# Kernel optimization log

Hardware: AMD Instinct MI355X
Metric: run time of the kernel (lower is better)

The kernel has to match this reference:

```python
import jax, jax.numpy as jnp
import numpy as np

B, L, DIM = 8, 512, 8          # batch, seq len, raw channels (value dim D = 2*DIM = 16)
ET, HID, H = 128, 128, 2       # embed_time, hidden_size, num_heads
MAXLEN = 512
NEG = -1e9


def setup_inputs() -> dict:
    key = jax.random.key(0)
    ks = jax.random.split(key, 40)
    def n(i, shape, s=0.05):
        return jax.random.normal(ks[i], shape, jnp.float32) * s
    vals = jax.random.normal(ks[0], (B, L, DIM), jnp.float32)
    msk = (jax.random.uniform(ks[1], (B, L, DIM)) > 0.2).astype(jnp.float32)
    x = jnp.concatenate([vals, msk], -1)                      # (B, L, 2*DIM)
    time_steps = jax.random.uniform(ks[2], (B, L), jnp.float32)
    return {
        'x': x, 'time_steps': time_steps,
        # learned time embedding: Linear(1, ET-1) periodic + Linear(1,1)
        'w_per': n(3, (1, ET - 1)), 'b_per': n(4, (ET - 1,)),
        'w_lin': n(5, (1, 1)), 'b_lin': n(6, (1,)),
        # MultiTimeAttention projections
        'Wq_t': n(7, (ET, ET)), 'bq_t': n(8, (ET,)),
        'Wk_t': n(9, (ET, ET)), 'bk_t': n(10, (ET,)),
        'Wo_t': n(11, (2 * DIM * H, HID)), 'bo_t': n(12, (HID,)),
        'pos_emb': n(13, (MAXLEN + 1, HID)), 'cls_emb': n(14, (1, HID)),
        # transformer block (BERT-style post-LN encoder layer, d_ff=HID)
        'tWq': n(15, (HID, HID)), 'tbq': n(16, (HID,)),
        'tWk': n(17, (HID, HID)), 'tbk': n(18, (HID,)),
        'tWv': n(19, (HID, HID)), 'tbv': n(20, (HID,)),
        'tWo': n(21, (HID, HID)), 'tbo': n(22, (HID,)),
        'ln1_g': jnp.ones((HID,), jnp.float32), 'ln1_b': jnp.zeros((HID,), jnp.float32),
        'fW1': n(23, (HID, HID)), 'fb1': n(24, (HID,)),
        'fW2': n(25, (HID, HID)), 'fb2': n(26, (HID,)),
        'ln2_g': jnp.ones((HID,), jnp.float32), 'ln2_b': jnp.zeros((HID,), jnp.float32),
        # BertPooler
        'pW': n(27, (HID, HID)), 'pb': n(28, (HID,)),
    }


def _time_emb(tt, w_per, b_per, w_lin, b_lin):
    tt = tt[..., None]                                        # (B, L, 1)
    return jnp.concatenate([tt @ w_lin + b_lin, jnp.sin(tt @ w_per + b_per)], -1)


def _ln(x, g, b, eps=1e-5):
    m = x.mean(-1, keepdims=True)
    v = ((x - m) ** 2).mean(-1, keepdims=True)
    return (x - m) / jnp.sqrt(v + eps) * g + b


def _mta(q_emb, k_emb, value, mask, Wq, bq, Wk, bk, Wo, bo):
    # MultiTimeAttention: scores broadcast to value-channel axis, softmax over keys
    D = value.shape[-1]
    dk = ET // H
    def split(e, W, b):
        p = e @ W + b
        return p.reshape(e.shape[0], -1, H, dk).transpose(0, 2, 1, 3)
    q = split(q_emb, Wq, bq)                                  # (Bq, H, Lq, dk)
    k = split(k_emb, Wk, bk)                                  # (B,  H, Lk, dk)
    scores = jnp.matmul(q, k.swapaxes(-1, -2)) / jnp.sqrt(jnp.float32(dk))  # (B,H,Lq,Lk)
    s5 = jnp.where(mask[:, None, None, :, :] == 0, NEG, scores[..., None])  # (B,H,Lq,Lk,D)
    p = jax.nn.softmax(s5, axis=-2)
    out = jnp.einsum('bhqkd,bkd->bhqd', p, value)             # (B, H, Lq, D)
    Bv = value.shape[0]
    out = out.transpose(0, 2, 1, 3).reshape(Bv, -1, H * D)
    return out @ Wo + bo


def _tblock(x, tWq, tbq, tWk, tbk, tWv, tbv, tWo, tbo, ln1_g, ln1_b,
            fW1, fb1, fW2, fb2, ln2_g, ln2_b):
    Bq, Lq, _ = x.shape
    dk = HID // H
    def heads(W, b):
        return (x @ W + b).reshape(Bq, Lq, H, dk).transpose(0, 2, 1, 3)
    q, k, v = heads(tWq, tbq), heads(tWk, tbk), heads(tWv, tbv)
    a = jax.nn.softmax(jnp.matmul(q, k.swapaxes(-1, -2)) / jnp.sqrt(jnp.float32(dk)), -1)
    o = jnp.matmul(a, v).transpose(0, 2, 1, 3).reshape(Bq, Lq, HID) @ tWo + tbo
    x = _ln(x + o, ln1_g, ln1_b)
    f = jax.nn.relu(x @ fW1 + fb1) @ fW2 + fb2
    return _ln(x + f, ln2_g, ln2_b)


def reference(x, time_steps, w_per, b_per, w_lin, b_lin,
              Wq_t, bq_t, Wk_t, bk_t, Wo_t, bo_t, pos_emb, cls_emb,
              tWq, tbq, tWk, tbk, tWv, tbv, tWo, tbo, ln1_g, ln1_b,
              fW1, fb1, fW2, fb2, ln2_g, ln2_b, pW, pb):
    Bx = x.shape[0]
    mask_half = x[:, :, DIM:]
    mask = jnp.concatenate([mask_half, mask_half], -1)        # (B, L, 2*DIM)
    key_e = _time_emb(time_steps, w_per, b_per, w_lin, b_lin)
    tq_e = _time_emb(time_steps, w_per, b_per, w_lin, b_lin)  # query_time_steps=None -> same
    cls_t = jnp.linspace(0.0, 1.0, 128, dtype=jnp.float32)[None]
    cls_q_e = _time_emb(cls_t, w_per, b_per, w_lin, b_lin)    # (1, 128, ET)
    cls_out = _mta(cls_q_e, key_e, x, mask, Wq_t, bq_t, Wk_t, bk_t, Wo_t, bo_t)
    out = _mta(tq_e, key_e, x, mask, Wq_t, bq_t, Wk_t, bk_t, Wo_t, bo_t)
    tb = (tWq, tbq, tWk, tbk, tWv, tbv, tWo, tbo, ln1_g, ln1_b,
          fW1, fb1, fW2, fb2, ln2_g, ln2_b)
    cls_repr = jnp.broadcast_to(cls_emb[None, :, :], (Bx, 1, HID))
    # encode(cls_out, is_pooling=True), pooling='bert': no pos emb, take token 0
    h = _tblock(jnp.concatenate([cls_repr, cls_out], 1), *tb)
    cls_pooling = jnp.tanh(h[:, 0] @ pW + pb)                 # (B, HID)
    # encode(out, is_pooling=False) [pretrain path]: pos emb + transformer, drop CLS
    h2 = jnp.concatenate([cls_repr, out], 1)                  # (B, L+1, HID)
    h2 = h2 + pos_emb[:h2.shape[1]][None]
    h2 = _tblock(h2, *tb)
    last_hidden_state = h2[:, 1:]                             # (B, L, HID)
    return cls_pooling, last_hidden_state
```

## Files before the change

kernel.cpp:

```cpp
#include <hip/hip_runtime.h>
#include <hip/hip_bf16.h>
#include <math.h>


static constexpr int NM_ = 8 * 513;
static constexpr int NC_ = 8 * 129;
static constexpr int NT_ = NM_ + NC_;

using bf = __hip_bfloat16;
typedef __attribute__((ext_vector_type(8))) short bf16x8;
typedef __attribute__((ext_vector_type(4))) short bf16x4;
typedef __attribute__((ext_vector_type(4))) float floatx4;
typedef __attribute__((ext_vector_type(8))) unsigned short ushortx8;

__device__ __forceinline__ float wave_reduce_sum(float v) {
    #pragma unroll
    for (int off = 32; off >= 1; off >>= 1) v += __shfl_xor(v, off);
    return v;
}
__device__ __forceinline__ float wave_reduce_max(float v) {
    #pragma unroll
    for (int off = 32; off >= 1; off >>= 1) v = fmaxf(v, __shfl_xor(v, off));
    return v;
}
__device__ __forceinline__ float u2f(unsigned short u) {
    return __uint_as_float(((unsigned)u) << 16);
}
__device__ __forceinline__ unsigned short f2u(float f) {
    unsigned u = __float_as_uint(f);
    return (unsigned short)((u + 0x7FFF + ((u >> 16) & 1)) >> 16);
}
__device__ __forceinline__ bf16x8 join8(bf16x4 lo, bf16x4 hi) {
    return __builtin_shufflevector(lo, hi, 0, 1, 2, 3, 4, 5, 6, 7);
}
__device__ __forceinline__ float rdin(const void* p, int i, int flag) {
    return flag ? u2f(((const unsigned short*)p)[i]) : ((const float*)p)[i];
}

struct PrepAll {
    const void* src[32]; int n[32]; int dstoff[32];
    int cstart[32]; int cnum[32];
    int ncv;
    const void* wsrc[8]; unsigned short* wdst[8]; float wscale[8];
    const void* ts; const void* w_per; const void* b_per;
    const void* w_lin; const void* b_lin;
    unsigned short* key_e16;
    unsigned short* btg;
    const void* xsrc;
    const unsigned short* det;
};
__global__ void prep_all_kernel(PrepAll a, float* dst) {
    int flag = (a.det[0] == 0x3F80u) ? 1 : 0;
    int blk = blockIdx.x, tid = threadIdx.x;
    if (blk < a.ncv) {
        int which = -1, bi = 0;
        #pragma unroll
        for (int i = 0; i < 32; ++i)
            if (blk >= a.cstart[i] && blk < a.cstart[i] + a.cnum[i]) { which = i; bi = blk - a.cstart[i]; }
        if (which < 0) return;
        int i = bi * 256 + tid;
        if (i < a.n[which]) dst[a.dstoff[which] + i] = rdin(a.src[which], i, flag);
    } else if (blk < a.ncv + 512) {
        int p = blk - a.ncv;
        int m = p >> 6;
        int idx = (p & 63) * 256 + tid;
        int c = idx >> 9;
        int l = (idx >> 3) & 63;
        int j = idx & 7;
        int k = (c >> 3) * 32 + (l >> 4) * 8 + j;
        int n = (c & 7) * 16 + (l & 15);
        a.wdst[m][idx] = f2u(rdin(a.wsrc[m], k * 128 + n, flag) * a.wscale[m]);
    } else if (blk < a.ncv + 512 + 2112) {
        int p = blk - a.ncv - 512;
        int row = p * 2 + (tid >> 7), j = tid & 127;
        float t = (row < 4096) ? rdin(a.ts, row, flag)
                               : (float)(row - 4096) * (1.0f / 127.0f);
        float v;
        if (j == 0) v = t * rdin(a.w_lin, 0, flag) + rdin(a.b_lin, 0, flag);
        else        v = sinf(t * rdin(a.w_per, j - 1, flag) + rdin(a.b_per, j - 1, flag));
        a.key_e16[row * 128 + j] = f2u(v);
    } else {
        int p = blk - a.ncv - 512 - 2112;
        int e0 = (p * 256 + tid) * 8;
        int b = e0 >> 13;
        int c = (e0 >> 9) & 15;
        int k0 = e0 & 511;
        unsigned short out[8];
        #pragma unroll
        for (int j = 0; j < 8; ++j) {
            int k = k0 + j;
            float m = rdin(a.xsrc, (b * 512 + k) * 16 + 8 + (c & 7), flag);
            float val = (c < 8) ? rdin(a.xsrc, (b * 512 + k) * 16 + c, flag) * m : m;
            out[j] = f2u(val);
        }
        *(ushortx8*)(a.btg + e0) = *(ushortx8*)out;
    }
}

struct GemmM {
    const void* A[3]; const unsigned short* W[3]; const float* bias[3];
    unsigned short* C[3];
    int M[3]; float bscale[3];
};
__global__ void __launch_bounds__(256)
gemm_mfma_kernel(GemmM p) {
    int y = blockIdx.y;
    const unsigned short* Wsw = p.W[y];
    const float* bias = p.bias[y];
    unsigned short* C = p.C[y];
    int M = p.M[y];
    float bscale = p.bscale[y];
    int m0 = blockIdx.x * 16;
    if (m0 >= M) return;
    __shared__ unsigned short As[16][136];
    int tid = threadIdx.x;
    {
        const unsigned short* A = (const unsigned short*)p.A[y];
        int r = tid >> 4, c0 = (tid & 15) * 8;
        ushortx8 v = {0, 0, 0, 0, 0, 0, 0, 0};
        if (m0 + r < M) v = *(const ushortx8*)(A + (size_t)(m0 + r) * 128 + c0);
        *(ushortx8*)&As[r][c0] = v;
    }
    __syncthreads();

    int wv = tid >> 6, lane = tid & 63;
    floatx4 acc0 = {0.f, 0.f, 0.f, 0.f}, acc1 = acc0;
    int am = lane & 15, aq = lane >> 4;
    #pragma unroll
    for (int ks = 0; ks < 4; ++ks) {
        bf16x8 af = *(bf16x8*)&As[am][ks * 32 + aq * 8];
        const unsigned short* base = Wsw + ((size_t)ks * 8 + 2 * wv) * 512 + lane * 8;
        bf16x8 b0 = *(const bf16x8*)(base);
        bf16x8 b1 = *(const bf16x8*)(base + 512);
        acc0 = __builtin_amdgcn_mfma_f32_16x16x32_bf16(af, b0, acc0, 0, 0, 0);
        acc1 = __builtin_amdgcn_mfma_f32_16x16x32_bf16(af, b1, acc1, 0, 0, 0);
    }
    int col = lane & 15, rowb = (lane >> 4) * 4;
    #pragma unroll
    for (int t = 0; t < 2; ++t) {
        floatx4 acc = t ? acc1 : acc0;
        int n = wv * 32 + t * 16 + col;
        float bv = bias[n] * bscale;
        #pragma unroll
        for (int rg = 0; rg < 4; ++rg) {
            int m = m0 + rowb + rg;
            if (m < M) C[(size_t)m * 128 + n] = f2u(acc[rg] + bv);
        }
    }
}

__global__ void __launch_bounds__(256)
mta_att_kernel(const unsigned short* qp_cls, const unsigned short* qp_main,
               const unsigned short* kp, const unsigned short* btg,
               float* att_cls, float* att_mn) {
    int F = blockIdx.x;
    int b = F & 7;
    int j = F >> 3;
    int h = j & 1;
    int xx = j >> 1;
    int is_cls = (xx >= 32);
    int qt = is_cls ? (xx - 32) : xx;
    int tid = threadIdx.x, lane = tid & 63, wv = tid >> 6;
    __shared__ unsigned short Qs[16][72];
    __shared__ unsigned short KV[64][72];
    __shared__ unsigned short sp[16][520];
    int q0 = qt * 16;

    if (tid < 128) {
        int r = tid >> 3, c0 = (tid & 7) * 8;
        const unsigned short* qrow = is_cls ? (qp_cls + (size_t)(q0 + r) * 128 + h * 64)
                                            : (qp_main + (size_t)(b * 512 + q0 + r) * 128 + h * 64);
        *(ushortx8*)&Qs[r][c0] = *(const ushortx8*)(qrow + c0);
    }
    __syncthreads();

    bf16x8 qf0, qf1;
    {
        int m = lane & 15, g = lane >> 4;
        qf0 = *(const bf16x8*)&Qs[m][g * 8];
        qf1 = *(const bf16x8*)&Qs[m][32 + g * 8];
    }

    for (int kt = 0; kt < 8; ++kt) {
        int k0 = kt * 64;
        {
            int kk = tid >> 3, e0 = (tid & 7) * 8;
            #pragma unroll
            for (int it = 0; it < 2; ++it, kk += 32)
                *(ushortx8*)&KV[kk][e0] =
                    *(const ushortx8*)(kp + (size_t)(b * 512 + k0 + kk) * 128 + h * 64 + e0);
        }
        __syncthreads();
        int kn = lane & 15, g = lane >> 4;
        floatx4 acc = {0.f, 0.f, 0.f, 0.f};
        {
            bf16x8 b0 = *(const bf16x8*)&KV[wv * 16 + kn][g * 8];
            acc = __builtin_amdgcn_mfma_f32_16x16x32_bf16(qf0, b0, acc, 0, 0, 0);
            bf16x8 b1 = *(const bf16x8*)&KV[wv * 16 + kn][32 + g * 8];
            acc = __builtin_amdgcn_mfma_f32_16x16x32_bf16(qf1, b1, acc, 0, 0, 0);
        }
        int colk = k0 + wv * 16 + kn;
        #pragma unroll
        for (int rg = 0; rg < 4; ++rg) sp[g * 4 + rg][colk] = f2u(acc[rg]);
        __syncthreads();
    }

    for (int rr = wv; rr < 16; rr += 4) {
        float m = -1e30f;
        for (int k = lane; k < 512; k += 64) m = fmaxf(m, u2f(sp[rr][k]));
        m = wave_reduce_max(m);
        for (int k = lane; k < 512; k += 64) sp[rr][k] = f2u(expf(u2f(sp[rr][k]) - m));
    }
    __syncthreads();

    floatx4 macc = {0.f, 0.f, 0.f, 0.f};
    {
        int mq = lane & 15, g = lane >> 4;
        const unsigned short* bbase = btg + ((size_t)(b * 16 + mq)) * 512 + g * 8;
        #pragma unroll
        for (int cc = 0; cc < 4; ++cc) {
            int koff = (wv + cc * 4) * 32;
            bf16x8 af = *(const bf16x8*)&sp[mq][koff + g * 8];
            bf16x8 bfv = *(const bf16x8*)(bbase + koff);
            macc = __builtin_amdgcn_mfma_f32_16x16x32_bf16(af, bfv, macc, 0, 0, 0);
        }
    }
    float* redC = (float*)&KV[0][0];
    float* Cfull = redC + 1024;
    #pragma unroll
    for (int rg = 0; rg < 4; ++rg) redC[(wv * 64 + lane) * 4 + rg] = macc[rg];
    __syncthreads();
    {
        int l = tid >> 2, rg = tid & 3;
        float s = redC[l * 4 + rg] + redC[(64 + l) * 4 + rg]
                + redC[(128 + l) * 4 + rg] + redC[(192 + l) * 4 + rg];
        int row = (l >> 4) * 4 + rg, c = l & 15;
        Cfull[row * 16 + c] = s;
    }
    __syncthreads();
    if (tid < 128) {
        int r = tid >> 3, c = tid & 7;
        float num = Cfull[r * 16 + c];
        float den = Cfull[r * 16 + 8 + c];
        int row = q0 + r;
        float* dst = is_cls ? (att_cls + (size_t)(b * 128 + row) * 32)
                            : (att_mn + (size_t)(b * 512 + row) * 32);
        dst[h * 16 + c] = num / den;
        dst[h * 16 + 8 + c] = 1.0f;
    }
}

__global__ void __launch_bounds__(256)
mta_qkv_kernel(const float* att, const float* Wo, const float* bo,
               const float* cls_emb, const float* pos, float* xin,
               const unsigned short* Wq, const unsigned short* Wk, const unsigned short* Wv,
               const float* bq, const float* bk, const float* bv_,
               unsigned short* outq, unsigned short* outk, unsigned short* outv) {
    int m0 = blockIdx.x * 16;
    __shared__ float As32[16][36];
    __shared__ unsigned short As[16][136];
    int tid = threadIdx.x;
    int r = tid >> 4, g = tid & 15, c0 = g * 8;

    int R = m0 + r;
    int srow, prow;
    if (R < NM_) {
        int b = R / 513, rr = R - b * 513;
        srow = (rr == 0) ? -1 : 1024 + b * 512 + (rr - 1);
        prow = rr;
    } else {
        int mc = R - NM_;
        int b = mc / 129, rr = mc - b * 129;
        srow = (rr == 0) ? -1 : b * 128 + (rr - 1);
        prow = -1;
    }
    if (g < 2 && srow >= 0) {
        const float* src = att + (size_t)srow * 32 + g * 16;
        *(float4*)&As32[r][g * 16]      = *(const float4*)(src);
        *(float4*)&As32[r][g * 16 + 4]  = *(const float4*)(src + 4);
        *(float4*)&As32[r][g * 16 + 8]  = *(const float4*)(src + 8);
        *(float4*)&As32[r][g * 16 + 12] = *(const float4*)(src + 12);
    }
    __syncthreads();

    float acc[8];
    if (srow < 0) {
        #pragma unroll
        for (int j = 0; j < 8; ++j) acc[j] = cls_emb[c0 + j];
    } else {
        #pragma unroll
        for (int j = 0; j < 8; ++j) acc[j] = bo[c0 + j];
        #pragma unroll 8
        for (int k = 0; k < 32; ++k) {
            float a = As32[r][k];
            const float4 w0 = *(const float4*)(Wo + (size_t)k * 128 + c0);
            const float4 w1 = *(const float4*)(Wo + (size_t)k * 128 + c0 + 4);
            acc[0] = fmaf(a, w0.x, acc[0]); acc[1] = fmaf(a, w0.y, acc[1]);
            acc[2] = fmaf(a, w0.z, acc[2]); acc[3] = fmaf(a, w0.w, acc[3]);
            acc[4] = fmaf(a, w1.x, acc[4]); acc[5] = fmaf(a, w1.y, acc[5]);
            acc[6] = fmaf(a, w1.z, acc[6]); acc[7] = fmaf(a, w1.w, acc[7]);
        }
    }
    if (prow >= 0) {
        const float* pr = pos + (size_t)prow * 128 + c0;
        float4 p0 = *(const float4*)(pr);
        float4 p1 = *(const float4*)(pr + 4);
        acc[0] += p0.x; acc[1] += p0.y; acc[2] += p0.z; acc[3] += p0.w;
        acc[4] += p1.x; acc[5] += p1.y; acc[6] += p1.z; acc[7] += p1.w;
    }
    *(float4*)(xin + (size_t)R * 128 + c0) = make_float4(acc[0], acc[1], acc[2], acc[3]);
    *(float4*)(xin + (size_t)R * 128 + c0 + 4) = make_float4(acc[4], acc[5], acc[6], acc[7]);
    *(ushort4*)&As[r][c0] = make_ushort4(f2u(acc[0]), f2u(acc[1]), f2u(acc[2]), f2u(acc[3]));
    *(ushort4*)&As[r][c0 + 4] = make_ushort4(f2u(acc[4]), f2u(acc[5]), f2u(acc[6]), f2u(acc[7]));
    __syncthreads();

    int wv = tid >> 6, lane = tid & 63;
    int am = lane & 15, aq = lane >> 4;
    int col = lane & 15, rowb = (lane >> 4) * 4;
    const unsigned short* Ws[3] = {Wq, Wk, Wv};
    const float* bs[3] = {bq, bk, bv_};
    float bsc[3] = {0.125f, 1.f, 1.f};
    unsigned short* Cs[3] = {outq, outk, outv};
    #pragma unroll
    for (int y = 0; y < 3; ++y) {
        floatx4 acc0 = {0.f, 0.f, 0.f, 0.f}, acc1 = acc0;
        #pragma unroll
        for (int ks = 0; ks < 4; ++ks) {
            bf16x8 af = *(bf16x8*)&As[am][ks * 32 + aq * 8];
            const unsigned short* base = Ws[y] + ((size_t)ks * 8 + 2 * wv) * 512 + lane * 8;
            bf16x8 b0 = *(const bf16x8*)(base);
            bf16x8 b1 = *(const bf16x8*)(base + 512);
            acc0 = __builtin_amdgcn_mfma_f32_16x16x32_bf16(af, b0, acc0, 0, 0, 0);
            acc1 = __builtin_amdgcn_mfma_f32_16x16x32_bf16(af, b1, acc1, 0, 0, 0);
        }
        #pragma unroll
        for (int t = 0; t < 2; ++t) {
            floatx4 a2 = t ? acc1 : acc0;
            int n = wv * 32 + t * 16 + col;
            float bvv = bs[y][n] * bsc[y];
            #pragma unroll
            for (int rg = 0; rg < 4; ++rg)
                Cs[y][(size_t)(m0 + rowb + rg) * 128 + n] = f2u(a2[rg] + bvv);
        }
    }
}

__global__ void __launch_bounds__(256)
tb_att_kernel(const unsigned short* qp, const unsigned short* kp,
              const unsigned short* vp, unsigned short* outp) {
    int F = blockIdx.x;
    int b = F & 7;
    int j = F >> 3;
    int h = j & 1;
    int xx = j >> 1;
    int is_cls = (xx >= 33);
    int qt = is_cls ? xx - 33 : xx;
    int Lq = is_cls ? 129 : 513;
    int base = is_cls ? (4104 + b * 129) : (b * 513);
    int nkt = is_cls ? 3 : 9;
    int tid = threadIdx.x, lane = tid & 63, wv = tid >> 6;
    __shared__ unsigned short Qs[16][72];
    __shared__ unsigned short KV[64][72];
    __shared__ unsigned short sp[16][588];
    __shared__ float rinv[16];
    int q0 = qt * 16;

    if (tid < 128) {
        int r = tid >> 3, c0 = (tid & 7) * 8;
        int qr = q0 + r;
        ushortx8 v = {0, 0, 0, 0, 0, 0, 0, 0};
        if (qr < Lq) v = *(const ushortx8*)(qp + (size_t)(base + qr) * 128 + h * 64 + c0);
        *(ushortx8*)&Qs[r][c0] = v;
    }
    __syncthreads();

    bf16x8 qf0, qf1;
    {
        int m = lane & 15, g = lane >> 4;
        qf0 = *(const bf16x8*)&Qs[m][g * 8];
        qf1 = *(const bf16x8*)&Qs[m][32 + g * 8];
    }

    for (int kt = 0; kt < nkt; ++kt) {
        int k0 = kt * 64;
        {
            int kk = tid >> 3, e0 = (tid & 7) * 8;
            #pragma unroll
            for (int it = 0; it < 2; ++it, kk += 32) {
                int krow = k0 + kk;
                ushortx8 v = {0, 0, 0, 0, 0, 0, 0, 0};
                if (krow < Lq) v = *(const ushortx8*)(kp + (size_t)(base + krow) * 128 + h * 64 + e0);
                *(ushortx8*)&KV[kk][e0] = v;
            }
        }
        __syncthreads();
        int kn = lane & 15, g = lane >> 4;
        floatx4 acc = {0.f, 0.f, 0.f, 0.f};
        {
            bf16x8 b0 = *(const bf16x8*)&KV[wv * 16 + kn][g * 8];
            acc = __builtin_amdgcn_mfma_f32_16x16x32_bf16(qf0, b0, acc, 0, 0, 0);
            bf16x8 b1 = *(const bf16x8*)&KV[wv * 16 + kn][32 + g * 8];
            acc = __builtin_amdgcn_mfma_f32_16x16x32_bf16(qf1, b1, acc, 0, 0, 0);
        }
        int colk = k0 + wv * 16 + kn;
        #pragma unroll
        for (int rg = 0; rg < 4; ++rg)
            sp[g * 4 + rg][colk] = f2u((colk < Lq) ? acc[rg] : -1e30f);
        __syncthreads();
    }

    int kend = nkt * 64;
    for (int rr = wv; rr < 16; rr += 4) {
        float m = -1e30f;
        for (int k = lane; k < kend; k += 64) m = fmaxf(m, u2f(sp[rr][k]));
        m = wave_reduce_max(m);
        float sum = 0.f;
        for (int k = lane; k < kend; k += 64) {
            float e = expf(u2f(sp[rr][k]) - m);
            sp[rr][k] = f2u(e);
            sum += e;
        }
        sum = wave_reduce_sum(sum);
        if (lane == 0) rinv[rr] = 1.f / sum;
    }

    floatx4 oacc = {0.f, 0.f, 0.f, 0.f};
    for (int kt = 0; kt < nkt; ++kt) {
        int k0 = kt * 64;
        __syncthreads();
        {
            int kk = tid & 31, e0 = (tid >> 5) * 8;
            #pragma unroll
            for (int it = 0; it < 2; ++it, kk += 32) {
                int krow = k0 + kk;
                ushortx8 v = {0, 0, 0, 0, 0, 0, 0, 0};
                if (krow < Lq) v = *(const ushortx8*)(vp + (size_t)(base + krow) * 128 + h * 64 + e0);
                #pragma unroll
                for (int j2 = 0; j2 < 8; ++j2) KV[e0 + j2][kk] = v[j2];
            }
        }
        __syncthreads();
        int dn = lane & 15, g = lane >> 4;
        #pragma unroll
        for (int c = 0; c < 2; ++c) {
            bf16x4 plo = *(const bf16x4*)&sp[lane & 15][k0 + c * 32 + g * 8];
            bf16x4 phi = *(const bf16x4*)&sp[lane & 15][k0 + c * 32 + g * 8 + 4];
            bf16x8 vf = *(const bf16x8*)&KV[wv * 16 + dn][c * 32 + g * 8];
            oacc = __builtin_amdgcn_mfma_f32_16x16x32_bf16(join8(plo, phi), vf, oacc, 0, 0, 0);
        }
    }
    int dcol = wv * 16 + (lane & 15), g = lane >> 4;
    #pragma unroll
    for (int rg = 0; rg < 4; ++rg) {
        int q = g * 4 + rg;
        int qr = q0 + q;
        if (qr < Lq)
            outp[(size_t)(base + qr) * 128 + h * 64 + dcol] = f2u(oacc[rg] * rinv[q]);
    }
}

__global__ void __launch_bounds__(256)
attnout_ffn_kernel(const unsigned short* A, const unsigned short* Wao, const float* bao,
                   const float* resid, const float* g1, const float* b1ln,
                   const unsigned short* W1, const float* fb1,
                   const unsigned short* W2, const float* fb2,
                   const float* g2, const float* b2ln,
                   const float* pW, const float* pb, float* dout) {
    int m0 = blockIdx.x * 16;
    __shared__ unsigned short As[16][136];
    __shared__ float Xs[16][128];
    __shared__ unsigned short Hs[16][136];
    __shared__ float redS[4][4][4], redQ[4][4][4];
    __shared__ float smean[16], sinv[16];
    __shared__ float x2row[128];
    __shared__ int poolb;
    int tid = threadIdx.x;
    if (tid == 0) poolb = -1;
    {
        int r = tid >> 4, c0 = (tid & 15) * 8;
        *(ushortx8*)&As[r][c0] = *(const ushortx8*)(A + (size_t)(m0 + r) * 128 + c0);
    }
    __syncthreads();

    int wv = tid >> 6, lane = tid & 63;
    int am = lane & 15, aq = lane >> 4;
    int col = lane & 15, g = lane >> 4, rowb = g * 4;

    float ov[2][4];
    {
        floatx4 acc0 = {0.f, 0.f, 0.f, 0.f}, acc1 = acc0;
        #pragma unroll
        for (int ks = 0; ks < 4; ++ks) {
            bf16x8 af = *(bf16x8*)&As[am][ks * 32 + aq * 8];
            const unsigned short* base = Wao + ((size_t)ks * 8 + 2 * wv) * 512 + lane * 8;
            bf16x8 bb0 = *(const bf16x8*)(base);
            bf16x8 bb1 = *(const bf16x8*)(base + 512);
            acc0 = __builtin_amdgcn_mfma_f32_16x16x32_bf16(af, bb0, acc0, 0, 0, 0);
            acc1 = __builtin_amdgcn_mfma_f32_16x16x32_bf16(af, bb1, acc1, 0, 0, 0);
        }
        #pragma unroll
        for (int t = 0; t < 2; ++t) {
            int n = wv * 32 + t * 16 + col;
            float bv = bao[n];
            floatx4 acc = t ? acc1 : acc0;
            #pragma unroll
            for (int rg = 0; rg < 4; ++rg)
                ov[t][rg] = acc[rg] + bv + resid[(size_t)(m0 + rowb + rg) * 128 + n];
        }
    }
    #pragma unroll
    for (int rg = 0; rg < 4; ++rg) {
        float s = ov[0][rg] + ov[1][rg];
        float q = ov[0][rg] * ov[0][rg] + ov[1][rg] * ov[1][rg];
        #pragma unroll
        for (int off = 8; off >= 1; off >>= 1) {
            s += __shfl_xor(s, off);
            q += __shfl_xor(q, off);
        }
        if ((lane & 15) == 0) { redS[wv][g][rg] = s; redQ[wv][g][rg] = q; }
    }
    __syncthreads();
    if (tid < 16) {
        int gg = tid >> 2, rg = tid & 3;
        float s = redS[0][gg][rg] + redS[1][gg][rg] + redS[2][gg][rg] + redS[3][gg][rg];
        float q = redQ[0][gg][rg] + redQ[1][gg][rg] + redQ[2][gg][rg] + redQ[3][gg][rg];
        float mean = s * 0.0078125f;
        float var = q * 0.0078125f - mean * mean;
        smean[tid] = mean;
        sinv[tid] = rsqrtf(var + 1e-5f);
    }
    __syncthreads();
    #pragma unroll
    for (int t = 0; t < 2; ++t) {
        int n = wv * 32 + t * 16 + col;
        float gm = g1[n], bb = b1ln[n];
        #pragma unroll
        for (int rg = 0; rg < 4; ++rg) {
            int row = rowb + rg;
            float val = (ov[t][rg] - smean[row]) * sinv[row] * gm + bb;
            Xs[row][n] = val;
            As[row][n] = f2u(val);
        }
    }
    __syncthreads();

    {
        floatx4 acc0 = {0.f, 0.f, 0.f, 0.f}, acc1 = acc0;
        #pragma unroll
        for (int ks = 0; ks < 4; ++ks) {
            bf16x8 af = *(bf16x8*)&As[am][ks * 32 + aq * 8];
            const unsigned short* base = W1 + ((size_t)ks * 8 + 2 * wv) * 512 + lane * 8;
            bf16x8 bb0 = *(const bf16x8*)(base);
            bf16x8 bb1 = *(const bf16x8*)(base + 512);
            acc0 = __builtin_amdgcn_mfma_f32_16x16x32_bf16(af, bb0, acc0, 0, 0, 0);
            acc1 = __builtin_amdgcn_mfma_f32_16x16x32_bf16(af, bb1, acc1, 0, 0, 0);
        }
        #pragma unroll
        for (int t = 0; t < 2; ++t) {
            int n = wv * 32 + t * 16 + col;
            float bv = fb1[n];
            floatx4 acc = t ? acc1 : acc0;
            #pragma unroll
            for (int rg = 0; rg < 4; ++rg)
                Hs[rowb + rg][n] = f2u(fmaxf(acc[rg] + bv, 0.f));
        }
    }
    __syncthreads();

    floatx4 acc0 = {0.f, 0.f, 0.f, 0.f}, acc1 = acc0;
    #pragma unroll
    for (int ks = 0; ks < 4; ++ks) {
        bf16x8 af = *(bf16x8*)&Hs[am][ks * 32 + aq * 8];
        const unsigned short* base = W2 + ((size_t)ks * 8 + 2 * wv) * 512 + lane * 8;
        bf16x8 bb0 = *(const bf16x8*)(base);
        bf16x8 bb1 = *(const bf16x8*)(base + 512);
        acc0 = __builtin_amdgcn_mfma_f32_16x16x32_bf16(af, bb0, acc0, 0, 0, 0);
        acc1 = __builtin_amdgcn_mfma_f32_16x16x32_bf16(af, bb1, acc1, 0, 0, 0);
    }
    #pragma unroll
    for (int t = 0; t < 2; ++t) {
        int n = wv * 32 + t * 16 + col;
        float bv = fb2[n];
        floatx4 acc = t ? acc1 : acc0;
        #pragma unroll
        for (int rg = 0; rg < 4; ++rg)
            ov[t][rg] = acc[rg] + bv + Xs[rowb + rg][n];
    }
    #pragma unroll
    for (int rg = 0; rg < 4; ++rg) {
        float s = ov[0][rg] + ov[1][rg];
        float q = ov[0][rg] * ov[0][rg] + ov[1][rg] * ov[1][rg];
        #pragma unroll
        for (int off = 8; off >= 1; off >>= 1) {
            s += __shfl_xor(s, off);
            q += __shfl_xor(q, off);
        }
        if ((lane & 15) == 0) { redS[wv][g][rg] = s; redQ[wv][g][rg] = q; }
    }
    __syncthreads();
    if (tid < 16) {
        int gg = tid >> 2, rg = tid & 3;
        float s = redS[0][gg][rg] + redS[1][gg][rg] + redS[2][gg][rg] + redS[3][gg][rg];
        float q = redQ[0][gg][rg] + redQ[1][gg][rg] + redQ[2][gg][rg] + redQ[3][gg][rg];
        float mean = s * 0.0078125f;
        float var = q * 0.0078125f - mean * mean;
        smean[tid] = mean;
        sinv[tid] = rsqrtf(var + 1e-5f);
    }
    __syncthreads();
    #pragma unroll
    for (int t = 0; t < 2; ++t) {
        int n = wv * 32 + t * 16 + col;
        float gm = g2[n], bb = b2ln[n];
        #pragma unroll
        for (int rg = 0; rg < 4; ++rg) {
            int row = rowb + rg;
            int m = m0 + row;
            float val = (ov[t][rg] - smean[row]) * sinv[row] * gm + bb;
            if (m < NM_) {
                int b = m / 513, r = m - b * 513;
                if (r >= 1)
                    dout[1024 + (size_t)b * 65536 + (size_t)(r - 1) * 128 + n] = val;
            } else {
                int mc = m - NM_;
                int b = mc / 129, r = mc - b * 129;
                if (r == 0) {
                    x2row[n] = val;
                    if (n == 0) poolb = b;
                }
            }
        }
    }
    __syncthreads();
    if (poolb >= 0 && tid < 128) {
        float acc = pb[tid];
        for (int k = 0; k < 128; ++k) acc = fmaf(x2row[k], pW[(size_t)k * 128 + tid], acc);
        dout[(size_t)poolb * 128 + tid] = tanhf(acc);
    }
}

extern "C" void kernel_launch(void* const* d_in, const int* in_sizes, int n_in,
                              void* d_out, int out_size, void* d_ws, size_t ws_size,
                              hipStream_t stream) {
    float* w = (float*)d_ws;
    size_t off = 0;
    auto alloc = [&](size_t n) {
        float* p = w + off;
        off += (n + 3) & ~(size_t)3;
        return p;
    };
    auto allocU = [&](size_t n) { return (unsigned short*)alloc((n + 1) / 2); };

    PrepAll pa{};
    int nn = n_in < 32 ? n_in : 32;
    float* fin[32];
    const int needconv[32] = {0,0,0,0,0,0, 0,1, 0,1, 1,1, 1,1, 0,1, 0,1, 0,1,
                              0,1, 1,1, 0,1, 0,1, 1,1, 1,1};
    int ncv = 0;
    for (int i = 0; i < nn; ++i) {
        pa.src[i] = d_in[i];
        pa.n[i] = in_sizes[i];
        fin[i] = alloc(in_sizes[i]);
        pa.dstoff[i] = (int)(fin[i] - w);
        if (needconv[i]) {
            int nb = (in_sizes[i] + 255) / 256;
            pa.cstart[i] = ncv;
            pa.cnum[i] = nb;
            ncv += nb;
        } else { pa.cstart[i] = -1; pa.cnum[i] = 0; }
    }
    for (int i = nn; i < 32; ++i) {
        pa.src[i] = nullptr; pa.n[i] = 0; pa.dstoff[i] = 0;
        pa.cstart[i] = -1; pa.cnum[i] = 0;
    }
    pa.ncv = ncv;

    const float* bq_t    = fin[7];
    const float* bk_t    = fin[9];
    const float* Wo_t    = fin[10]; const float* bo_t = fin[11];
    const float* pos_emb = fin[12]; const float* cls_emb = fin[13];
    const float* tbq = fin[15]; const float* tbk = fin[17]; const float* tbv = fin[19];
    const float* tbo = fin[21];
    const float* ln1_g = fin[22]; const float* ln1_b = fin[23];
    const float* fb1 = fin[25]; const float* fb2 = fin[27];
    const float* ln2_g = fin[28]; const float* ln2_b = fin[29];
    const float* pW = fin[30]; const float* pb = fin[31];

    const int widx[8] = {8, 6, 14, 16, 18, 20, 24, 26};
    unsigned short* wsw[8];
    for (int i = 0; i < 8; ++i) {
        wsw[i] = allocU(16384);
        pa.wsrc[i] = d_in[widx[i]];
        pa.wdst[i] = wsw[i];
        pa.wscale[i] = (i == 1 || i == 2) ? 0.125f : 1.0f;
    }
    pa.ts = d_in[1]; pa.w_per = d_in[2]; pa.b_per = d_in[3];
    pa.w_lin = d_in[4]; pa.b_lin = d_in[5];
    pa.xsrc = d_in[0];
    pa.det = (const unsigned short*)d_in[22];

    unsigned short* key_e16 = allocU(4224 * 128);
    unsigned short* cls_e16 = key_e16 + 4096 * 128;
    pa.key_e16 = key_e16;
    unsigned short* btg = allocU(8 * 16 * 512);
    pa.btg = btg;

    unsigned short* qp_main16 = allocU(4096 * 128);
    unsigned short* kp_main16 = allocU(4096 * 128);
    unsigned short* qp_cls16  = allocU(128 * 128);
    float* att_all = alloc(5120 * 32);
    float* att_cls = att_all;
    float* att_mn  = att_all + 1024 * 32;
    float* xin     = alloc((size_t)NT_ * 128);
    unsigned short* tbq16 = allocU((size_t)NT_ * 128);
    unsigned short* tbk16 = allocU((size_t)NT_ * 128);
    unsigned short* tbv16 = allocU((size_t)NT_ * 128);
    unsigned short* tba16 = allocU((size_t)NT_ * 128);
    (void)ws_size;

    float* outf = (float*)d_out;

    prep_all_kernel<<<ncv + 512 + 2112 + 32, 256, 0, stream>>>(pa, w);

    {
        GemmM p{};
        p.A[0] = key_e16; p.W[0] = wsw[0]; p.bias[0] = bk_t; p.C[0] = kp_main16;
        p.M[0] = 4096; p.bscale[0] = 1.f;
        p.A[1] = key_e16; p.W[1] = wsw[1]; p.bias[1] = bq_t; p.C[1] = qp_main16;
        p.M[1] = 4096; p.bscale[1] = 0.125f;
        p.A[2] = cls_e16; p.W[2] = wsw[1]; p.bias[2] = bq_t; p.C[2] = qp_cls16;
        p.M[2] = 128; p.bscale[2] = 0.125f;
        gemm_mfma_kernel<<<dim3(256, 3), 256, 0, stream>>>(p);
    }

    mta_att_kernel<<<640, 256, 0, stream>>>(qp_cls16, qp_main16, kp_main16,
                                            btg, att_cls, att_mn);

    mta_qkv_kernel<<<321, 256, 0, stream>>>(att_all, Wo_t, bo_t, cls_emb, pos_emb, xin,
                                            wsw[2], wsw[3], wsw[4], tbq, tbk, tbv,
                                            tbq16, tbk16, tbv16);

    tb_att_kernel<<<672, 256, 0, stream>>>(tbq16, tbk16, tbv16, tba16);

    attnout_ffn_kernel<<<321, 256, 0, stream>>>(tba16, wsw[5], tbo, xin, ln1_g, ln1_b,
                                                wsw[6], fb1, wsw[7], fb2, ln2_g, ln2_b,
                                                pW, pb, outf);
}
```

Measured before the change: 186.1 us.

## Split attention key range across blocks and merge partial softmax in consumer kernels

Both attention kernels now divide the key dimension into chunks (2 for the time attention, 3 for the transformer attention), and each block writes unnormalized partial outputs plus row max and sum. The following kernels (mta_qkv and attnout_ffn) combine the partials with a flash-decoding style log-sum-exp merge before their GEMMs. This doubles or nearly triples the block count to improve occupancy and parallelism on the wide GPU and shrinks shared-memory score buffers. The cost is extra fp32 partial-result traffic through global memory and redundant Q loads per chunk.

```diff
diff --git a/kernel.cpp b/kernel.cpp
--- a/kernel.cpp
+++ b/kernel.cpp
@@ -150,12 +150,14 @@
 }
 
 __global__ void __launch_bounds__(256)
-mta_att_kernel(const unsigned short* qp_cls, const unsigned short* qp_main,
-               const unsigned short* kp, const unsigned short* btg,
-               float* att_cls, float* att_mn) {
+mta_att_part_kernel(const unsigned short* qp_cls, const unsigned short* qp_main,
+                    const unsigned short* kp, const unsigned short* btg,
+                    float* mpa, float* mma) {
     int F = blockIdx.x;
     int b = F & 7;
-    int j = F >> 3;
+    int j2 = F >> 3;
+    int ch = j2 & 1;
+    int j = j2 >> 1;
     int h = j & 1;
     int xx = j >> 1;
     int is_cls = (xx >= 32);
@@ -163,8 +165,10 @@
     int tid = threadIdx.x, lane = tid & 63, wv = tid >> 6;
     __shared__ unsigned short Qs[16][72];
     __shared__ unsigned short KV[64][72];
-    __shared__ unsigned short sp[16][520];
+    __shared__ unsigned short sp[16][264];
+    __shared__ float mrow[16];
     int q0 = qt * 16;
+    int kg0 = ch * 256;
 
     if (tid < 128) {
         int r = tid >> 3, c0 = (tid & 7) * 8;
@@ -181,14 +185,14 @@
         qf1 = *(const bf16x8*)&Qs[m][32 + g * 8];
     }
 
-    for (int kt = 0; kt < 8; ++kt) {
+    for (int kt = 0; kt < 4; ++kt) {
         int k0 = kt * 64;
         {
             int kk = tid >> 3, e0 = (tid & 7) * 8;
             #pragma unroll
             for (int it = 0; it < 2; ++it, kk += 32)
                 *(ushortx8*)&KV[kk][e0] =
-                    *(const ushortx8*)(kp + (size_t)(b * 512 + k0 + kk) * 128 + h * 64 + e0);
+                    *(const ushortx8*)(kp + (size_t)(b * 512 + kg0 + k0 + kk) * 128 + h * 64 + e0);
         }
         __syncthreads();
         int kn = lane & 15, g = lane >> 4;
@@ -207,18 +211,19 @@
 
     for (int rr = wv; rr < 16; rr += 4) {
         float m = -1e30f;
-        for (int k = lane; k < 512; k += 64) m = fmaxf(m, u2f(sp[rr][k]));
+        for (int k = lane; k < 256; k += 64) m = fmaxf(m, u2f(sp[rr][k]));
         m = wave_reduce_max(m);
-        for (int k = lane; k < 512; k += 64) sp[rr][k] = f2u(expf(u2f(sp[rr][k]) - m));
+        for (int k = lane; k < 256; k += 64) sp[rr][k] = f2u(expf(u2f(sp[rr][k]) - m));
+        if (lane == 0) mrow[rr] = m;
     }
     __syncthreads();
 
     floatx4 macc = {0.f, 0.f, 0.f, 0.f};
     {
         int mq = lane & 15, g = lane >> 4;
-        const unsigned short* bbase = btg + ((size_t)(b * 16 + mq)) * 512 + g * 8;
-        #pragma unroll
-        for (int cc = 0; cc < 4; ++cc) {
+        const unsigned short* bbase = btg + ((size_t)(b * 16 + mq)) * 512 + kg0 + g * 8;
+        #pragma unroll
+        for (int cc = 0; cc < 2; ++cc) {
             int koff = (wv + cc * 4) * 32;
             bf16x8 af = *(const bf16x8*)&sp[mq][koff + g * 8];
             bf16x8 bfv = *(const bf16x8*)(bbase + koff);
@@ -238,20 +243,14 @@
         Cfull[row * 16 + c] = s;
     }
     __syncthreads();
-    if (tid < 128) {
-        int r = tid >> 3, c = tid & 7;
-        float num = Cfull[r * 16 + c];
-        float den = Cfull[r * 16 + 8 + c];
-        int row = q0 + r;
-        float* dst = is_cls ? (att_cls + (size_t)(b * 128 + row) * 32)
-                            : (att_mn + (size_t)(b * 512 + row) * 32);
-        dst[h * 16 + c] = num / den;
-        dst[h * 16 + 8 + c] = 1.0f;
-    }
+    size_t pidx = ((size_t)(((b * 2 + h) * 40) + xx)) * 2 + ch;
+    mpa[pidx * 256 + tid] = Cfull[tid];
+    if (tid < 16) mma[pidx * 16 + tid] = mrow[tid];
 }
 
 __global__ void __launch_bounds__(256)
-mta_qkv_kernel(const float* att, const float* Wo, const float* bo,
+mta_qkv_kernel(const float* mpa, const float* mma,
+               const float* Wo, const float* bo,
                const float* cls_emb, const float* pos, float* xin,
                const unsigned short* Wq, const unsigned short* Wk, const unsigned short* Wv,
                const float* bq, const float* bk, const float* bv_,
@@ -266,20 +265,36 @@
     int srow, prow;
     if (R < NM_) {
         int b = R / 513, rr = R - b * 513;
-        srow = (rr == 0) ? -1 : 1024 + b * 512 + (rr - 1);
+        srow = (rr == 0) ? -1 : 1;
         prow = rr;
     } else {
         int mc = R - NM_;
         int b = mc / 129, rr = mc - b * 129;
-        srow = (rr == 0) ? -1 : b * 128 + (rr - 1);
+        srow = (rr == 0) ? -1 : 1;
         prow = -1;
     }
-    if (g < 2 && srow >= 0) {
-        const float* src = att + (size_t)srow * 32 + g * 16;
-        *(float4*)&As32[r][g * 16]      = *(const float4*)(src);
-        *(float4*)&As32[r][g * 16 + 4]  = *(const float4*)(src + 4);
-        *(float4*)&As32[r][g * 16 + 8]  = *(const float4*)(src + 8);
-        *(float4*)&As32[r][g * 16 + 12] = *(const float4*)(src + 12);
+    if (srow >= 0) {
+        int hh = g >> 3, c = g & 7;
+        int bb, xx2, lr2;
+        if (R < NM_) {
+            bb = R / 513; int ridx = R - bb * 513 - 1;
+            xx2 = ridx >> 4; lr2 = ridx & 15;
+        } else {
+            int mc = R - NM_;
+            bb = mc / 129; int ridx = mc - bb * 129 - 1;
+            xx2 = 32 + (ridx >> 4); lr2 = ridx & 15;
+        }
+        size_t p0 = ((size_t)(((bb * 2 + hh) * 40) + xx2)) * 2;
+        const float* C0 = mpa + (p0 + 0) * 256 + lr2 * 16;
+        const float* C1 = mpa + (p0 + 1) * 256 + lr2 * 16;
+        float m0v = mma[(p0 + 0) * 16 + lr2];
+        float m1v = mma[(p0 + 1) * 16 + lr2];
+        float mm = fmaxf(m0v, m1v);
+        float e0 = expf(m0v - mm), e1 = expf(m1v - mm);
+        float num = C0[c] * e0 + C1[c] * e1;
+        float den = C0[8 + c] * e0 + C1[8 + c] * e1;
+        As32[r][hh * 16 + c] = num / den;
+        As32[r][hh * 16 + 8 + c] = 1.0f;
     }
     __syncthreads();
 
@@ -346,24 +361,27 @@
 }
 
 __global__ void __launch_bounds__(256)
-tb_att_kernel(const unsigned short* qp, const unsigned short* kp,
-              const unsigned short* vp, unsigned short* outp) {
+tb_att_part_kernel(const unsigned short* qp, const unsigned short* kp,
+                   const unsigned short* vp,
+                   float* opm, float* mlm, float* opc, float* mlc) {
     int F = blockIdx.x;
     int b = F & 7;
-    int j = F >> 3;
-    int h = j & 1;
-    int xx = j >> 1;
-    int is_cls = (xx >= 33);
-    int qt = is_cls ? xx - 33 : xx;
+    int j2 = F >> 3;
+    int h = j2 & 1;
+    int t = j2 >> 1;
+    int is_cls = (t >= 99);
+    int qt, ch;
+    if (is_cls) { qt = t - 99; ch = 0; }
+    else        { qt = t / 3;  ch = t - qt * 3; }
     int Lq = is_cls ? 129 : 513;
     int base = is_cls ? (4104 + b * 129) : (b * 513);
-    int nkt = is_cls ? 3 : 9;
     int tid = threadIdx.x, lane = tid & 63, wv = tid >> 6;
     __shared__ unsigned short Qs[16][72];
     __shared__ unsigned short KV[64][72];
-    __shared__ unsigned short sp[16][588];
-    __shared__ float rinv[16];
+    __shared__ unsigned short sp[16][200];
+    __shared__ float mrow[16], lrow[16];
     int q0 = qt * 16;
+    int kg0 = ch * 192;
 
     if (tid < 128) {
         int r = tid >> 3, c0 = (tid & 7) * 8;
@@ -381,13 +399,14 @@
         qf1 = *(const bf16x8*)&Qs[m][32 + g * 8];
     }
 
-    for (int kt = 0; kt < nkt; ++kt) {
+    #pragma unroll
+    for (int kt = 0; kt < 3; ++kt) {
         int k0 = kt * 64;
         {
             int kk = tid >> 3, e0 = (tid & 7) * 8;
             #pragma unroll
             for (int it = 0; it < 2; ++it, kk += 32) {
-                int krow = k0 + kk;
+                int krow = kg0 + k0 + kk;
                 ushortx8 v = {0, 0, 0, 0, 0, 0, 0, 0};
                 if (krow < Lq) v = *(const ushortx8*)(kp + (size_t)(base + krow) * 128 + h * 64 + e0);
                 *(ushortx8*)&KV[kk][e0] = v;
@@ -405,38 +424,40 @@
         int colk = k0 + wv * 16 + kn;
         #pragma unroll
         for (int rg = 0; rg < 4; ++rg)
-            sp[g * 4 + rg][colk] = f2u((colk < Lq) ? acc[rg] : -1e30f);
+            sp[g * 4 + rg][colk] = f2u((kg0 + colk < Lq) ? acc[rg] : -1e30f);
         __syncthreads();
     }
 
-    int kend = nkt * 64;
     for (int rr = wv; rr < 16; rr += 4) {
         float m = -1e30f;
-        for (int k = lane; k < kend; k += 64) m = fmaxf(m, u2f(sp[rr][k]));
+        #pragma unroll
+        for (int k = 0; k < 3; ++k) m = fmaxf(m, u2f(sp[rr][k * 64 + lane]));
         m = wave_reduce_max(m);
         float sum = 0.f;
-        for (int k = lane; k < kend; k += 64) {
-            float e = expf(u2f(sp[rr][k]) - m);
-            sp[rr][k] = f2u(e);
+        #pragma unroll
+        for (int k = 0; k < 3; ++k) {
+            float e = expf(u2f(sp[rr][k * 64 + lane]) - m);
+            sp[rr][k * 64 + lane] = f2u(e);
             sum += e;
         }
         sum = wave_reduce_sum(sum);
-        if (lane == 0) rinv[rr] = 1.f / sum;
+        if (lane == 0) { mrow[rr] = m; lrow[rr] = sum; }
     }
 
     floatx4 oacc = {0.f, 0.f, 0.f, 0.f};
-    for (int kt = 0; kt < nkt; ++kt) {
+    #pragma unroll
+    for (int kt = 0; kt < 3; ++kt) {
         int k0 = kt * 64;
         __syncthreads();
         {
             int kk = tid & 31, e0 = (tid >> 5) * 8;
             #pragma unroll
             for (int it = 0; it < 2; ++it, kk += 32) {
-                int krow = k0 + kk;
+                int krow = kg0 + k0 + kk;
                 ushortx8 v = {0, 0, 0, 0, 0, 0, 0, 0};
                 if (krow < Lq) v = *(const ushortx8*)(vp + (size_t)(base + krow) * 128 + h * 64 + e0);
                 #pragma unroll
-                for (int j2 = 0; j2 < 8; ++j2) KV[e0 + j2][kk] = v[j2];
+                for (int j3 = 0; j3 < 8; ++j3) KV[e0 + j3][kk] = v[j3];
             }
         }
         __syncthreads();
@@ -449,18 +470,26 @@
             oacc = __builtin_amdgcn_mfma_f32_16x16x32_bf16(join8(plo, phi), vf, oacc, 0, 0, 0);
         }
     }
+    float* op = is_cls ? (opc + ((size_t)((b * 2 + h) * 9 + qt)) * 1024)
+                       : (opm + ((size_t)(((b * 2 + h) * 33 + qt) * 3 + ch)) * 1024);
     int dcol = wv * 16 + (lane & 15), g = lane >> 4;
     #pragma unroll
     for (int rg = 0; rg < 4; ++rg) {
         int q = g * 4 + rg;
-        int qr = q0 + q;
-        if (qr < Lq)
-            outp[(size_t)(base + qr) * 128 + h * 64 + dcol] = f2u(oacc[rg] * rinv[q]);
+        op[q * 64 + dcol] = oacc[rg];
+    }
+    if (tid < 16) {
+        float* ml = is_cls ? (mlc + ((size_t)((b * 2 + h) * 9 + qt)) * 32)
+                           : (mlm + ((size_t)(((b * 2 + h) * 33 + qt) * 3 + ch)) * 32);
+        ml[tid * 2]     = mrow[tid];
+        ml[tid * 2 + 1] = lrow[tid];
     }
 }
 
 __global__ void __launch_bounds__(256)
-attnout_ffn_kernel(const unsigned short* A, const unsigned short* Wao, const float* bao,
+attnout_ffn_kernel(const float* opm, const float* mlm,
+                   const float* opc, const float* mlc,
+                   const unsigned short* Wao, const float* bao,
                    const float* resid, const float* g1, const float* b1ln,
                    const unsigned short* W1, const float* fb1,
                    const unsigned short* W2, const float* fb2,
@@ -478,7 +507,41 @@
     if (tid == 0) poolb = -1;
     {
         int r = tid >> 4, c0 = (tid & 15) * 8;
-        *(ushortx8*)&As[r][c0] = *(const ushortx8*)(A + (size_t)(m0 + r) * 128 + c0);
+        int R = m0 + r;
+        int iscl, bb, rr;
+        if (R < NM_) { bb = R / 513; rr = R - bb * 513; iscl = 0; }
+        else { int mc = R - NM_; bb = mc / 129; rr = mc - bb * 129; iscl = 1; }
+        int qt = rr >> 4, lr = rr & 15;
+        int hh = c0 >> 6, d0 = c0 & 63;
+        float vals[8];
+        if (iscl) {
+            size_t pb2 = (size_t)((bb * 2 + hh) * 9 + qt);
+            const float* op = opc + pb2 * 1024 + lr * 64 + d0;
+            float linv = 1.f / mlc[pb2 * 32 + lr * 2 + 1];
+            #pragma unroll
+            for (int jj = 0; jj < 8; ++jj) vals[jj] = op[jj] * linv;
+        } else {
+            size_t pb2 = (size_t)(((bb * 2 + hh) * 33 + qt) * 3);
+            const float* op0 = opm + (pb2 + 0) * 1024 + lr * 64 + d0;
+            const float* op1 = opm + (pb2 + 1) * 1024 + lr * 64 + d0;
+            const float* op2 = opm + (pb2 + 2) * 1024 + lr * 64 + d0;
+            float m0v = mlm[(pb2 + 0) * 32 + lr * 2];
+            float m1v = mlm[(pb2 + 1) * 32 + lr * 2];
+            float m2v = mlm[(pb2 + 2) * 32 + lr * 2];
+            float l0 = mlm[(pb2 + 0) * 32 + lr * 2 + 1];
+            float l1 = mlm[(pb2 + 1) * 32 + lr * 2 + 1];
+            float l2 = mlm[(pb2 + 2) * 32 + lr * 2 + 1];
+            float mm = fmaxf(fmaxf(m0v, m1v), m2v);
+            float e0 = expf(m0v - mm), e1 = expf(m1v - mm), e2 = expf(m2v - mm);
+            float linv = 1.f / (l0 * e0 + l1 * e1 + l2 * e2);
+            #pragma unroll
+            for (int jj = 0; jj < 8; ++jj)
+                vals[jj] = (op0[jj] * e0 + op1[jj] * e1 + op2[jj] * e2) * linv;
+        }
+        unsigned short o8[8];
+        #pragma unroll
+        for (int jj = 0; jj < 8; ++jj) o8[jj] = f2u(vals[jj]);
+        *(ushortx8*)&As[r][c0] = *(ushortx8*)o8;
     }
     __syncthreads();
 
@@ -618,13 +681,13 @@
             int m = m0 + row;
             float val = (ov[t][rg] - smean[row]) * sinv[row] * gm + bb;
             if (m < NM_) {
-                int b = m / 513, r = m - b * 513;
-                if (r >= 1)
-                    dout[1024 + (size_t)b * 65536 + (size_t)(r - 1) * 128 + n] = val;
+                int b = m / 513, r2 = m - b * 513;
+                if (r2 >= 1)
+                    dout[1024 + (size_t)b * 65536 + (size_t)(r2 - 1) * 128 + n] = val;
             } else {
                 int mc = m - NM_;
-                int b = mc / 129, r = mc - b * 129;
-                if (r == 0) {
+                int b = mc / 129, r2 = mc - b * 129;
+                if (r2 == 0) {
                     x2row[n] = val;
                     if (n == 0) poolb = b;
                 }
@@ -708,14 +771,16 @@
     unsigned short* qp_main16 = allocU(4096 * 128);
     unsigned short* kp_main16 = allocU(4096 * 128);
     unsigned short* qp_cls16  = allocU(128 * 128);
-    float* att_all = alloc(5120 * 32);
-    float* att_cls = att_all;
-    float* att_mn  = att_all + 1024 * 32;
-    float* xin     = alloc((size_t)NT_ * 128);
+    float* mpa = alloc(1280 * 256);
+    float* mma = alloc(1280 * 16);
+    float* opm = alloc((size_t)1584 * 1024);
+    float* mlm = alloc(1584 * 32);
+    float* opc = alloc((size_t)144 * 1024);
+    float* mlc = alloc(144 * 32);
+    float* xin = alloc((size_t)NT_ * 128);
     unsigned short* tbq16 = allocU((size_t)NT_ * 128);
     unsigned short* tbk16 = allocU((size_t)NT_ * 128);
     unsigned short* tbv16 = allocU((size_t)NT_ * 128);
-    unsigned short* tba16 = allocU((size_t)NT_ * 128);
     (void)ws_size;
 
     float* outf = (float*)d_out;
@@ -733,16 +798,18 @@
         gemm_mfma_kernel<<<dim3(256, 3), 256, 0, stream>>>(p);
     }
 
-    mta_att_kernel<<<640, 256, 0, stream>>>(qp_cls16, qp_main16, kp_main16,
-                                            btg, att_cls, att_mn);
-
-    mta_qkv_kernel<<<321, 256, 0, stream>>>(att_all, Wo_t, bo_t, cls_emb, pos_emb, xin,
+    mta_att_part_kernel<<<1280, 256, 0, stream>>>(qp_cls16, qp_main16, kp_main16,
+                                                  btg, mpa, mma);
+
+    mta_qkv_kernel<<<321, 256, 0, stream>>>(mpa, mma, Wo_t, bo_t, cls_emb, pos_emb, xin,
                                             wsw[2], wsw[3], wsw[4], tbq, tbk, tbv,
                                             tbq16, tbk16, tbv16);
 
-    tb_att_kernel<<<672, 256, 0, stream>>>(tbq16, tbk16, tbv16, tba16);
-
-    attnout_ffn_kernel<<<321, 256, 0, stream>>>(tba16, wsw[5], tbo, xin, ln1_g, ln1_b,
+    tb_att_part_kernel<<<1728, 256, 0, stream>>>(tbq16, tbk16, tbv16,
+                                                 opm, mlm, opc, mlc);
+
+    attnout_ffn_kernel<<<321, 256, 0, stream>>>(opm, mlm, opc, mlc,
+                                                wsw[5], tbo, xin, ln1_g, ln1_b,
                                                 wsw[6], fb1, wsw[7], fb2, ln2_g, ln2_b,
                                                 pW, pb, outf);
 }
```

Result: faster. 179.5 us (-3.5%).
